# Kernel optimization log

Measured on AMD Instinct MI355X. Metric: run time of the kernel, lower is better.

## Reference

```python
import jax, jax.numpy as jnp
import numpy as np

D_MODEL = 1024
NUM_HEADS = 4
KEY_DIM = 1024      # dim * expand_k
VALUE_DIM = 2048    # dim * expand_v
HEAD_QK = KEY_DIM // NUM_HEADS   # 256
HEAD_V = VALUE_DIM // NUM_HEADS  # 512
EPS = 1e-5
ROPE_BASE = 10000.0
XAVIER_GAIN = 2.0 ** (-2.5)


def _xavier_uniform(key, shape, gain=XAVIER_GAIN):
    fan_in, fan_out = shape
    a = gain * np.sqrt(6.0 / (fan_in + fan_out))
    return jax.random.uniform(key, shape, jnp.float32, -a, a)


def setup_inputs() -> dict:
    key = jax.random.key(0)
    ks = jax.random.split(key, 5)
    x = jax.random.normal(ks[0], (2, 2048, D_MODEL), jnp.float32)
    # stored as (in, out); y = x @ W matches torch Linear(no bias) with W^T
    Wq = _xavier_uniform(ks[1], (D_MODEL, KEY_DIM))
    Wk = _xavier_uniform(ks[2], (D_MODEL, KEY_DIM))
    Wv = _xavier_uniform(ks[3], (D_MODEL, VALUE_DIM))
    Wo = _xavier_uniform(ks[4], (VALUE_DIM, D_MODEL))
    return {"x": x, "Wq": Wq, "Wk": Wk, "Wv": Wv, "Wo": Wo}


def _rope(t, base=ROPE_BASE):
    # t: [b, n, h, d]; standard half-split rotary embedding
    n, d = t.shape[1], t.shape[-1]
    half = d // 2
    inv_freq = 1.0 / (base ** (jnp.arange(0, half, dtype=jnp.float32) * 2.0 / d))
    ang = jnp.arange(n, dtype=jnp.float32)[:, None] * inv_freq  # [n, d/2]
    cos = jnp.cos(ang)[None, :, None, :]
    sin = jnp.sin(ang)[None, :, None, :]
    t1, t2 = t[..., :half], t[..., half:]
    return jnp.concatenate([t1 * cos - t2 * sin, t2 * cos + t1 * sin], axis=-1)


def reference(x, Wq, Wk, Wv, Wo):
    b, n, _ = x.shape
    # projections: b n (h d) -> b (n) h d
    q = (x @ Wq).reshape(b, n, NUM_HEADS, HEAD_QK)
    k = (x @ Wk).reshape(b, n, NUM_HEADS, HEAD_QK)
    v = (x @ Wv).reshape(b, n, NUM_HEADS, HEAD_V).transpose(0, 2, 1, 3)  # b h n dv
    q = _rope(q).transpose(0, 2, 1, 3)  # b h n dk
    k = _rope(k).transpose(0, 2, 1, 3)
    scale = HEAD_QK ** (-0.5)
    exp_qk = jnp.tril(jnp.exp(jnp.einsum('bhid,bhjd->bhij', q, k) * scale))
    exp_kk = jnp.tril(jnp.exp(jnp.einsum('bhid,bhjd->bhij', k, k) * scale))
    A = exp_kk.astype(jnp.float32) + EPS * jnp.eye(n, dtype=jnp.float32)
    sol = jax.lax.linalg.triangular_solve(A, v.astype(jnp.float32),
                                          left_side=True, lower=True)
    o = exp_qk.astype(jnp.float32) @ sol                # b h n dv
    o = o.transpose(0, 2, 1, 3).reshape(b, n, VALUE_DIM)  # b n (h dv)
    return o.astype(x.dtype) @ Wo
```

## Files before the change

kernel.cpp:

```cpp
#include <hip/hip_runtime.h>
#include <hip/hip_bf16.h>
#include <math.h>

#define SEQ   2048
#define NROW  4096
#define DM    1024
#define LDQ   1024
#define LDV   2048
#define NBLK  16

typedef float  f32x4  __attribute__((ext_vector_type(4)));
typedef int    i32x4  __attribute__((ext_vector_type(4)));
typedef __bf16 bf16x8 __attribute__((ext_vector_type(8)));

#define MFMA(d, a, b) (d) = __builtin_amdgcn_mfma_f32_16x16x32_bf16((a), (b), (d), 0, 0, 0)

__device__ inline ushort f2bf(float f) {
  __hip_bfloat16 h = __float2bfloat16(f);
  return *(ushort*)&h;
}
__device__ inline float bf2f(ushort u) {
  return __uint_as_float((unsigned)u << 16);
}
__device__ inline void split2(float v, ushort& hi, ushort& lo) {
  hi = f2bf(v);
  lo = f2bf(v - bf2f(hi));
}
__device__ inline bf16x8 ldfrag(const ushort* p) { return *(const bf16x8*)p; }

__device__ inline void gload_lds16(const ushort* g, ushort* l) {
  __builtin_amdgcn_global_load_lds(
      (const __attribute__((address_space(1))) void*)g,
      (__attribute__((address_space(3))) void*)l, 16, 0, 0);
}

__global__ void pack_x_kernel(const float* __restrict__ X, ushort* __restrict__ P)
{
  const int t = blockIdx.x * 256 + threadIdx.x;
  const int kc = t & 127;
  const int m  = t >> 7;
  const float* src = X + (size_t)m * DM + kc * 8;
  f32x4 v0 = *(const f32x4*)src;
  f32x4 v1 = *(const f32x4*)(src + 4);
  ushort o[8];
  #pragma unroll
  for (int j = 0; j < 4; ++j) { o[j] = f2bf(v0[j]); o[4 + j] = f2bf(v1[j]); }
  ushort* dst = P + ((size_t)((m >> 7) * 128 + kc) * 128 + (m & 127)) * 8;
  *(i32x4*)dst = *(i32x4*)o;
}

__global__ void pack_w_kernel(const float* __restrict__ W, ushort* __restrict__ P,
                              int K, int N)
{
  const int K8 = K >> 3;
  const int t = blockIdx.x * 256 + threadIdx.x;
  const int c  = t & 127;
  const int kc = (t >> 7) % K8;
  const int nb = t / (128 * K8);
  ushort o[8];
  #pragma unroll
  for (int j = 0; j < 8; ++j)
    o[j] = f2bf(W[(size_t)(kc * 8 + j) * N + nb * 128 + c]);
  ushort* dst = P + ((size_t)(nb * K8 + kc) * 128 + c) * 8;
  *(i32x4*)dst = *(i32x4*)o;
}

__global__ void rope_pack1_kernel(const float* __restrict__ M,
                                  ushort* __restrict__ Phi, ushort* __restrict__ Plo)
{
  const int idx = blockIdx.x * 256 + threadIdx.x;
  const int g   = idx & 31;
  const int h   = (idx >> 5) & 3;
  const int row = idx >> 7;
  const int pos = row & (SEQ - 1);
  const int d0  = g * 8;
  const bool hihalf = d0 >= 128;
  const int f0 = d0 & 127;
  const float* mp = M + (size_t)row * LDQ + h * 256;
  ushort oh[8], ol[8];
  #pragma unroll
  for (int j = 0; j < 8; ++j) {
    const int f = f0 + j;
    const float inv = expf(-(float)f * (9.210340371976184f / 128.f));
    float s, c;
    sincosf((float)pos * inv, &s, &c);
    const float m1 = mp[f], m2 = mp[f + 128];
    const float mv = hihalf ? (m2 * c + m1 * s) : (m1 * c - m2 * s);
    split2(mv, oh[j], ol[j]);
  }
  const int b = row >> 11, r = row & 127, tb = (row & 2047) >> 7;
  const int bh = b * 4 + h;
  const size_t doff = (((size_t)(bh * 16 + tb) * 32 + g) * 128 + r) * 8;
  *(i32x4*)(Phi + doff) = *(i32x4*)oh;
  *(i32x4*)(Plo + doff) = *(i32x4*)ol;
}

__global__ void pack_sol_kernel(const float* __restrict__ Vb, ushort* __restrict__ Sp)
{
  const int hj = blockIdx.x;
  const int h  = hj >> 4, jb = hj & 15;
  const int c  = blockIdx.y * 256 + threadIdx.x;
  const float* src = Vb + (size_t)(jb * 128) * LDV + h * 512 + c;
  ushort* dhi = Sp + ((size_t)hj * 2    ) * 65536;
  ushort* dlo = Sp + ((size_t)hj * 2 + 1) * 65536;
  for (int kc = 0; kc < 16; ++kc) {
    ushort oh[8], ol[8];
    #pragma unroll
    for (int j = 0; j < 8; ++j)
      split2(src[(size_t)(kc * 8 + j) * LDV], oh[j], ol[j]);
    *(i32x4*)(dhi + ((size_t)kc * 512 + c) * 8) = *(i32x4*)oh;
    *(i32x4*)(dlo + ((size_t)kc * 512 + c) * 8) = *(i32x4*)ol;
  }
}

__global__ __launch_bounds__(256) void gemm_bf16(
    const ushort* __restrict__ Ap, const ushort* __restrict__ Bp,
    float* __restrict__ C, int M, int N, int K)
{
  __shared__ __align__(16) ushort a_lds[8][128][8];
  __shared__ __align__(16) ushort b_lds[8][128][8];
  const int tid  = threadIdx.x;
  const int lane = tid & 63;
  const int w    = tid >> 6;
  const int wr   = w >> 1, wc = w & 1;
  const int mb = blockIdx.y, nb = blockIdx.x;
  const int K8 = K >> 3;
  const ushort* aT = Ap + (size_t)mb * K8 * 1024;
  const ushort* bT = Bp + (size_t)nb * K8 * 1024;
  const int lr = lane & 15;
  const int lk = lane >> 4;

  f32x4 acc[4][4];
  #pragma unroll
  for (int i = 0; i < 4; ++i)
    #pragma unroll
    for (int j = 0; j < 4; ++j) acc[i][j] = (f32x4)(0.f);

  for (int kc0 = 0; kc0 < K8; kc0 += 8) {
    const ushort* asrc = aT + (size_t)kc0 * 1024;
    const ushort* bsrc = bT + (size_t)kc0 * 1024;
    __syncthreads();
    #pragma unroll
    for (int it = 0; it < 4; ++it) {
      gload_lds16(asrc + it * 2048 + tid * 8, ((ushort*)a_lds) + it * 2048 + tid * 8);
      gload_lds16(bsrc + it * 2048 + tid * 8, ((ushort*)b_lds) + it * 2048 + tid * 8);
    }
    __syncthreads();
    #pragma unroll
    for (int kk = 0; kk < 2; ++kk) {
      bf16x8 af[4], bf[4];
      #pragma unroll
      for (int m = 0; m < 4; ++m)
        af[m] = ldfrag(&a_lds[kk * 4 + lk][wr * 64 + m * 16 + lr][0]);
      #pragma unroll
      for (int n = 0; n < 4; ++n)
        bf[n] = ldfrag(&b_lds[kk * 4 + lk][wc * 64 + n * 16 + lr][0]);
      #pragma unroll
      for (int m = 0; m < 4; ++m)
        #pragma unroll
        for (int n = 0; n < 4; ++n)
          MFMA(acc[m][n], af[m], bf[n]);
    }
  }
  const int r0 = (lane >> 4) * 4;
  #pragma unroll
  for (int m = 0; m < 4; ++m)
    #pragma unroll
    for (int n = 0; n < 4; ++n) {
      const int row = mb * 128 + wr * 64 + m * 16 + r0;
      const int col = nb * 128 + wc * 64 + n * 16 + lr;
      float* cp = C + (size_t)row * N + col;
      #pragma unroll
      for (int q = 0; q < 4; ++q) cp[(size_t)q * N] = acc[m][n][q];
    }
}

__global__ __launch_bounds__(256) void winv_kernel(
    const ushort* __restrict__ Khi, const ushort* __restrict__ Klo,
    ushort* __restrict__ Whi, ushort* __restrict__ Wlo)
{
  __shared__ float L[128][129];
  __shared__ float W[128][129];
  const int t = blockIdx.x, bh = blockIdx.y;
  const int tid = threadIdx.x;
  const int lane = tid & 63, w = tid >> 6;
  const int wr = w >> 1, wc = w & 1;
  const int lr = lane & 15, lk = lane >> 4;
  const size_t kb = (size_t)(bh * 16 + t) * 32768;

  f32x4 acc[4][4];
  #pragma unroll
  for (int i = 0; i < 4; ++i)
    #pragma unroll
    for (int j = 0; j < 4; ++j) acc[i][j] = (f32x4)(0.f);
  #pragma unroll
  for (int ks = 0; ks < 8; ++ks) {
    bf16x8 ah[4], al[4];
    #pragma unroll
    for (int m = 0; m < 4; ++m) {
      const size_t off = kb + ((size_t)(ks * 4 + lk) * 128 + wr * 64 + m * 16 + lr) * 8;
      ah[m] = ldfrag(Khi + off);
      al[m] = ldfrag(Klo + off);
    }
    #pragma unroll
    for (int n = 0; n < 4; ++n) {
      const size_t off = kb + ((size_t)(ks * 4 + lk) * 128 + wc * 64 + n * 16 + lr) * 8;
      bf16x8 bh_ = ldfrag(Khi + off);
      bf16x8 bl_ = ldfrag(Klo + off);
      #pragma unroll
      for (int m = 0; m < 4; ++m) {
        MFMA(acc[m][n], ah[m], bh_);
        MFMA(acc[m][n], ah[m], bl_);
        MFMA(acc[m][n], al[m], bh_);
      }
    }
  }
  for (int i = tid; i < 128 * 129; i += 256) ((float*)W)[i] = 0.f;
  #pragma unroll
  for (int m = 0; m < 4; ++m)
    #pragma unroll
    for (int n = 0; n < 4; ++n)
      #pragma unroll
      for (int q = 0; q < 4; ++q) {
        const int row = wr * 64 + m * 16 + lk * 4 + q;
        const int col = wc * 64 + n * 16 + lr;
        float v = __expf(acc[m][n][q] * 0.0625f);
        if (row == col) v += 1e-5f;
        L[row][col] = v;
      }
  __syncthreads();
  if (tid < 128) {
    const int c = tid;
    W[c][c] = 1.f / L[c][c];
    for (int r = c + 1; r < 128; ++r) {
      float s0 = 0.f, s1 = 0.f, s2 = 0.f, s3 = 0.f;
      int j = c;
      for (; j + 4 <= r; j += 4) {
        s0 += L[r][j]     * W[j][c];
        s1 += L[r][j + 1] * W[j + 1][c];
        s2 += L[r][j + 2] * W[j + 2][c];
        s3 += L[r][j + 3] * W[j + 3][c];
      }
      for (; j < r; ++j) s0 += L[r][j] * W[j][c];
      W[r][c] = -((s0 + s1) + (s2 + s3)) / L[r][r];
    }
  }
  __syncthreads();
  const size_t wb = (size_t)(bh * 16 + t) * 16384;
  for (int i = tid; i < 2048; i += 256) {
    const int kc = i >> 7, r = i & 127;
    ushort oh[8], ol[8];
    #pragma unroll
    for (int j = 0; j < 8; ++j) split2(W[r][kc * 8 + j], oh[j], ol[j]);
    *(i32x4*)(Whi + wb + (size_t)i * 8) = *(i32x4*)oh;
    *(i32x4*)(Wlo + wb + (size_t)i * 8) = *(i32x4*)ol;
  }
}

__global__ __launch_bounds__(512) void apply_w0_kernel(
    const ushort* __restrict__ Whi, const ushort* __restrict__ Wlo,
    float* __restrict__ V, ushort* __restrict__ SR)
{
  __shared__ __align__(16) ushort shi[16 * 128 * 8];
  __shared__ __align__(16) ushort slo[16 * 128 * 8];
  const int cc = blockIdx.x, bh = blockIdx.y;
  const int b = bh >> 2, h = bh & 3;
  const int tid = threadIdx.x;
  const int lane = tid & 63, w = tid >> 6;
  const int wr = w >> 2, wc = w & 3, lr = lane & 15, lk = lane >> 4;
  const size_t wb = (size_t)(bh * 16) * 16384;
  float* Vrows = V + (size_t)b * SEQ * LDV + h * 512;
  ushort* srw = SR + (size_t)bh * 131072;

  {
    const int k = tid >> 2, c0 = (tid & 3) * 32;
    const float* vp = Vrows + (size_t)k * LDV + cc * 128 + c0;
    for (int c = 0; c < 32; ++c) {
      ushort hi, lo;
      split2(vp[c], hi, lo);
      const int idx = (((k >> 3) * 128) + c0 + c) * 8 + (k & 7);
      shi[idx] = hi; slo[idx] = lo;
    }
  }
  __syncthreads();
  f32x4 acc[4][2];
  #pragma unroll
  for (int i = 0; i < 4; ++i)
    #pragma unroll
    for (int j = 0; j < 2; ++j) acc[i][j] = (f32x4)(0.f);
  #pragma unroll
  for (int ks = 0; ks < 4; ++ks) {
    bf16x8 ah[4], al[4];
    #pragma unroll
    for (int m = 0; m < 4; ++m) {
      const size_t off = wb + ((size_t)(ks * 4 + lk) * 128 + wr * 64 + m * 16 + lr) * 8;
      ah[m] = ldfrag(Whi + off);
      al[m] = ldfrag(Wlo + off);
    }
    #pragma unroll
    for (int n = 0; n < 2; ++n) {
      const int idx = (((ks * 4 + lk) * 128) + wc * 32 + n * 16 + lr) * 8;
      bf16x8 bh_ = ldfrag(&shi[idx]);
      bf16x8 bl_ = ldfrag(&slo[idx]);
      #pragma unroll
      for (int m = 0; m < 4; ++m) {
        MFMA(acc[m][n], ah[m], bh_);
        MFMA(acc[m][n], ah[m], bl_);
        MFMA(acc[m][n], al[m], bh_);
      }
    }
  }
  #pragma unroll
  for (int m = 0; m < 4; ++m)
    #pragma unroll
    for (int n = 0; n < 2; ++n) {
      const int col = wc * 32 + n * 16 + lr;
      #pragma unroll
      for (int q = 0; q < 4; ++q) {
        const int row = wr * 64 + m * 16 + lk * 4 + q;
        const float v = acc[m][n][q];
        Vrows[(size_t)row * LDV + cc * 128 + col] = v;
        ushort hi, lo;
        split2(v, hi, lo);
        const size_t so = ((size_t)(row >> 3) * 512 + cc * 128 + col) * 8 + (row & 7);
        srw[so] = hi; srw[65536 + so] = lo;
      }
    }
}

__global__ __launch_bounds__(512) void solve_step_kernel(
    const ushort* __restrict__ Khi, const ushort* __restrict__ Klo,
    const ushort* __restrict__ Whi, const ushort* __restrict__ Wlo,
    float* __restrict__ V, ushort* __restrict__ SR, int t)
{
  __shared__ __align__(16) ushort pAhi[16 * 128 * 8];
  __shared__ __align__(16) ushort pAlo[16 * 128 * 8];
  const int ib = t + 1 + blockIdx.x;
  const int cc = blockIdx.y;
  const int bh = blockIdx.z;
  const int b = bh >> 2, h = bh & 3;
  const bool lead = (blockIdx.x == 0);
  const int tid = threadIdx.x;
  const int lane = tid & 63, w = tid >> 6;
  const int wr = w >> 2, wc = w & 3, lr = lane & 15, lk = lane >> 4;
  const size_t kbi = (size_t)(bh * 16 + ib) * 32768;
  const size_t kbt = (size_t)(bh * 16 + t) * 32768;
  float* Vhead = V + (size_t)b * SEQ * LDV + h * 512;
  float* Vib = Vhead + (size_t)ib * 128 * LDV;
  const ushort* srr = SR + (size_t)(t & 1) * 1048576 + (size_t)bh * 131072;
  ushort* srw       = SR + (size_t)((t + 1) & 1) * 1048576 + (size_t)bh * 131072;

  {
    f32x4 a1[4][2];
    #pragma unroll
    for (int i = 0; i < 4; ++i)
      #pragma unroll
      for (int j = 0; j < 2; ++j) a1[i][j] = (f32x4)(0.f);
    #pragma unroll
    for (int ks = 0; ks < 8; ++ks) {
      bf16x8 ah[4], al[4];
      #pragma unroll
      for (int m = 0; m < 4; ++m) {
        const size_t off = kbi + ((size_t)(ks * 4 + lk) * 128 + wr * 64 + m * 16 + lr) * 8;
        ah[m] = ldfrag(Khi + off);
        al[m] = ldfrag(Klo + off);
      }
      #pragma unroll
      for (int n = 0; n < 2; ++n) {
        const size_t off = kbt + ((size_t)(ks * 4 + lk) * 128 + wc * 32 + n * 16 + lr) * 8;
        bf16x8 bh_ = ldfrag(Khi + off);
        bf16x8 bl_ = ldfrag(Klo + off);
        #pragma unroll
        for (int m = 0; m < 4; ++m) {
          MFMA(a1[m][n], ah[m], bh_);
          MFMA(a1[m][n], ah[m], bl_);
          MFMA(a1[m][n], al[m], bh_);
        }
      }
    }
    #pragma unroll
    for (int m = 0; m < 4; ++m)
      #pragma unroll
      for (int n = 0; n < 2; ++n)
        #pragma unroll
        for (int q = 0; q < 4; ++q) {
          const int row = wr * 64 + m * 16 + lk * 4 + q;
          const int c   = wc * 32 + n * 16 + lr;
          const float e = __expf(a1[m][n][q] * 0.0625f);
          ushort hi, lo;
          split2(e, hi, lo);
          const int idx = (((c >> 3) * 128) + row) * 8 + (c & 7);
          pAhi[idx] = hi; pAlo[idx] = lo;
        }
  }
  __syncthreads();

  f32x4 u[4][2];
  #pragma unroll
  for (int i = 0; i < 4; ++i)
    #pragma unroll
    for (int j = 0; j < 2; ++j) u[i][j] = (f32x4)(0.f);
  #pragma unroll
  for (int ks = 0; ks < 4; ++ks) {
    bf16x8 ah[4], al[4];
    #pragma unroll
    for (int m = 0; m < 4; ++m) {
      const int idx = (((ks * 4 + lk) * 128) + wr * 64 + m * 16 + lr) * 8;
      ah[m] = ldfrag(&pAhi[idx]);
      al[m] = ldfrag(&pAlo[idx]);
    }
    #pragma unroll
    for (int n = 0; n < 2; ++n) {
      const size_t c = cc * 128 + wc * 32 + n * 16 + lr;
      bf16x8 bh_ = ldfrag(srr + ((size_t)(ks * 4 + lk) * 512 + c) * 8);
      bf16x8 bl_ = ldfrag(srr + 65536 + ((size_t)(ks * 4 + lk) * 512 + c) * 8);
      #pragma unroll
      for (int m = 0; m < 4; ++m) {
        MFMA(u[m][n], ah[m], bh_);
        MFMA(u[m][n], ah[m], bl_);
        MFMA(u[m][n], al[m], bh_);
      }
    }
  }
  float nv[4][2][4];
  #pragma unroll
  for (int m = 0; m < 4; ++m)
    #pragma unroll
    for (int n = 0; n < 2; ++n) {
      const int col = wc * 32 + n * 16 + lr;
      #pragma unroll
      for (int q = 0; q < 4; ++q) {
        const int row = wr * 64 + m * 16 + lk * 4 + q;
        const float v = Vib[(size_t)row * LDV + cc * 128 + col] - u[m][n][q];
        nv[m][n][q] = v;
        if (!lead) Vib[(size_t)row * LDV + cc * 128 + col] = v;
      }
    }
  if (lead) {
    __syncthreads();
    #pragma unroll
    for (int m = 0; m < 4; ++m)
      #pragma unroll
      for (int n = 0; n < 2; ++n) {
        const int col = wc * 32 + n * 16 + lr;
        #pragma unroll
        for (int q = 0; q < 4; ++q) {
          const int row = wr * 64 + m * 16 + lk * 4 + q;
          ushort hi, lo;
          split2(nv[m][n][q], hi, lo);
          const int idx = (((row >> 3) * 128) + col) * 8 + (row & 7);
          pAhi[idx] = hi; pAlo[idx] = lo;
        }
      }
    __syncthreads();
    f32x4 s2[4][2];
    #pragma unroll
    for (int i = 0; i < 4; ++i)
      #pragma unroll
      for (int j = 0; j < 2; ++j) s2[i][j] = (f32x4)(0.f);
    const size_t wb = (size_t)(bh * 16 + ib) * 16384;
    #pragma unroll
    for (int ks = 0; ks < 4; ++ks) {
      bf16x8 ah[4], al[4];
      #pragma unroll
      for (int m = 0; m < 4; ++m) {
        const size_t off = wb + ((size_t)(ks * 4 + lk) * 128 + wr * 64 + m * 16 + lr) * 8;
        ah[m] = ldfrag(Whi + off);
        al[m] = ldfrag(Wlo + off);
      }
      #pragma unroll
      for (int n = 0; n < 2; ++n) {
        const int idx = (((ks * 4 + lk) * 128) + wc * 32 + n * 16 + lr) * 8;
        bf16x8 bh_ = ldfrag(&pAhi[idx]);
        bf16x8 bl_ = ldfrag(&pAlo[idx]);
        #pragma unroll
        for (int m = 0; m < 4; ++m) {
          MFMA(s2[m][n], ah[m], bh_);
          MFMA(s2[m][n], ah[m], bl_);
          MFMA(s2[m][n], al[m], bh_);
        }
      }
    }
    #pragma unroll
    for (int m = 0; m < 4; ++m)
      #pragma unroll
      for (int n = 0; n < 2; ++n) {
        const int col = wc * 32 + n * 16 + lr;
        #pragma unroll
        for (int q = 0; q < 4; ++q) {
          const int row = wr * 64 + m * 16 + lk * 4 + q;
          const float v = s2[m][n][q];
          Vib[(size_t)row * LDV + cc * 128 + col] = v;
          ushort hi, lo;
          split2(v, hi, lo);
          const size_t so = ((size_t)(row >> 3) * 512 + cc * 128 + col) * 8 + (row & 7);
          srw[so] = hi; srw[65536 + so] = lo;
        }
      }
  }
}

__global__ __launch_bounds__(512, 4) void o_kernel(
    const ushort* __restrict__ Qhi, const ushort* __restrict__ Qlo,
    const ushort* __restrict__ Khi, const ushort* __restrict__ Klo,
    const ushort* __restrict__ Sp0, const ushort* __restrict__ Sp1,
    ushort* __restrict__ Opack)
{
  __shared__ __align__(16) ushort Phi_s[16 * 64 * 8];
  __shared__ __align__(16) ushort Plo_s[16 * 64 * 8];
  const int bid = blockIdx.x;
  const int bh  = bid & 7;
  const int t3  = bid >> 3;
  const int ch  = t3 & 1;
  const int rh  = (t3 >> 1) & 1;
  const int ib  = 15 - (t3 >> 2);
  const int b = bh >> 2, h = bh & 3;
  const int tid = threadIdx.x;
  const int lane = tid & 63, w = tid >> 6;
  const int wr = w >> 2, wc = w & 3, lr = lane & 15, lk = lane >> 4;
  const ushort* Spb = b ? Sp1 : Sp0;

  const size_t qb = (size_t)(bh * 16 + ib) * 32768;
  f32x4 acc[2][4];
  #pragma unroll
  for (int i = 0; i < 2; ++i)
    #pragma unroll
    for (int j = 0; j < 4; ++j) acc[i][j] = (f32x4)(0.f);

  for (int jb = 0; jb <= ib; ++jb) {
    f32x4 s1[2][2];
    #pragma unroll
    for (int i = 0; i < 2; ++i)
      #pragma unroll
      for (int j = 0; j < 2; ++j) s1[i][j] = (f32x4)(0.f);
    const size_t kb = (size_t)(bh * 16 + jb) * 32768;
    __builtin_amdgcn_s_setprio(1);
    #pragma unroll
    for (int ks = 0; ks < 8; ++ks) {
      bf16x8 ah[2], al[2];
      #pragma unroll
      for (int m = 0; m < 2; ++m) {
        const size_t off = qb + ((size_t)(ks * 4 + lk) * 128 + rh * 64 + wr * 32 + m * 16 + lr) * 8;
        ah[m] = ldfrag(Qhi + off);
        al[m] = ldfrag(Qlo + off);
      }
      #pragma unroll
      for (int n = 0; n < 2; ++n) {
        const size_t off = kb + ((size_t)(ks * 4 + lk) * 128 + wc * 32 + n * 16 + lr) * 8;
        bf16x8 bh_ = ldfrag(Khi + off);
        bf16x8 bl_ = ldfrag(Klo + off);
        #pragma unroll
        for (int m = 0; m < 2; ++m) {
          MFMA(s1[m][n], ah[m], bh_);
          MFMA(s1[m][n], ah[m], bl_);
          MFMA(s1[m][n], al[m], bh_);
        }
      }
    }
    __builtin_amdgcn_s_setprio(0);
    if (jb) __syncthreads();
    #pragma unroll
    for (int m = 0; m < 2; ++m)
      #pragma unroll
      for (int n = 0; n < 2; ++n)
        #pragma unroll
        for (int q = 0; q < 4; ++q) {
          const int rloc = wr * 32 + m * 16 + lk * 4 + q;
          const int c    = wc * 32 + n * 16 + lr;
          float e = __expf(s1[m][n][q] * 0.0625f);
          if (jb == ib && c > rh * 64 + rloc) e = 0.f;
          ushort hi, lo;
          split2(e, hi, lo);
          const int idx = (((c >> 3) * 64) + rloc) * 8 + (c & 7);
          Phi_s[idx] = hi; Plo_s[idx] = lo;
        }
    __syncthreads();
    const ushort* sjb = Spb + ((size_t)(h * 16 + jb) * 2) * 65536;
    __builtin_amdgcn_s_setprio(1);
    #pragma unroll
    for (int ks = 0; ks < 4; ++ks) {
      bf16x8 ah[2], al[2];
      #pragma unroll
      for (int m = 0; m < 2; ++m) {
        const int idx = (((ks * 4 + lk) * 64) + wr * 32 + m * 16 + lr) * 8;
        ah[m] = ldfrag(&Phi_s[idx]);
        al[m] = ldfrag(&Plo_s[idx]);
      }
      #pragma unroll
      for (int n = 0; n < 4; ++n) {
        const size_t c = ch * 256 + wc * 64 + n * 16 + lr;
        bf16x8 bh_ = ldfrag(sjb + ((size_t)(ks * 4 + lk) * 512 + c) * 8);
        bf16x8 bl_ = ldfrag(sjb + 65536 + ((size_t)(ks * 4 + lk) * 512 + c) * 8);
        #pragma unroll
        for (int m = 0; m < 2; ++m) {
          MFMA(acc[m][n], ah[m], bh_);
          MFMA(acc[m][n], ah[m], bl_);
          MFMA(acc[m][n], al[m], bh_);
        }
      }
    }
    __builtin_amdgcn_s_setprio(0);
  }
  const int row_blk = b * 16 + ib;
  #pragma unroll
  for (int m = 0; m < 2; ++m)
    #pragma unroll
    for (int n = 0; n < 4; ++n) {
      const int col = h * 512 + ch * 256 + wc * 64 + n * 16 + lr;
      #pragma unroll
      for (int q = 0; q < 4; ++q) {
        const int row = rh * 64 + wr * 32 + m * 16 + lk * 4 + q;
        Opack[((size_t)row_blk * 256 + (col >> 3)) * 1024 + row * 8 + (col & 7)] =
            f2bf(acc[m][n][q]);
      }
    }
}

extern "C" void kernel_launch(void* const* d_in, const int* in_sizes, int n_in,
                              void* d_out, int out_size, void* d_ws, size_t ws_size,
                              hipStream_t stream)
{
  const float* x  = (const float*)d_in[0];
  const float* Wq = (const float*)d_in[1];
  const float* Wk = (const float*)d_in[2];
  const float* Wv = (const float*)d_in[3];
  const float* Wo = (const float*)d_in[4];
  float* out = (float*)d_out;

  char* base = (char*)d_ws;
  ushort* xpack = (ushort*)(base);
  ushort* Wqp   = (ushort*)(base + (8u  << 20));
  ushort* Wkp   = (ushort*)(base + (10u << 20));
  ushort* Wvp   = (ushort*)(base + (12u << 20));
  ushort* Wop   = (ushort*)(base + (16u << 20));
  float*  Q     = (float*) (base + (20u << 20));
  float*  K     = (float*) (base + (36u << 20));
  float*  V     = (float*) (base + (52u << 20));
  ushort* Qhi   = (ushort*)(base);
  ushort* Qlo   = (ushort*)(base + (8u  << 20));
  ushort* Khi   = (ushort*)(base + (20u << 20));
  ushort* Klo   = (ushort*)(base + (28u << 20));
  ushort* Whi   = (ushort*)(base + (36u << 20));
  ushort* Wlo   = (ushort*)(base + (40u << 20));
  ushort* SR    = (ushort*)(base + (44u << 20));
  ushort* Sp1   = (ushort*)(base + (36u << 20));
  ushort* Sp0   = (ushort*)(base + (68u << 20));
  ushort* Opack = (ushort*)(base + (52u << 20));

  pack_x_kernel<<<(NROW * 128) / 256, 256, 0, stream>>>(x, xpack);
  pack_w_kernel<<<(1024 * 1024 / 8) / 256, 256, 0, stream>>>(Wq, Wqp, 1024, 1024);
  pack_w_kernel<<<(1024 * 1024 / 8) / 256, 256, 0, stream>>>(Wk, Wkp, 1024, 1024);
  pack_w_kernel<<<(1024 * 2048 / 8) / 256, 256, 0, stream>>>(Wv, Wvp, 1024, 2048);
  pack_w_kernel<<<(2048 * 1024 / 8) / 256, 256, 0, stream>>>(Wo, Wop, 2048, 1024);

  gemm_bf16<<<dim3(DM / 128, NROW / 128), 256, 0, stream>>>(xpack, Wqp, Q, NROW, DM, DM);
  gemm_bf16<<<dim3(DM / 128, NROW / 128), 256, 0, stream>>>(xpack, Wkp, K, NROW, DM, DM);
  gemm_bf16<<<dim3(LDV / 128, NROW / 128), 256, 0, stream>>>(xpack, Wvp, V, NROW, LDV, DM);

  rope_pack1_kernel<<<(NROW * 4 * 32) / 256, 256, 0, stream>>>(Q, Qhi, Qlo);
  rope_pack1_kernel<<<(NROW * 4 * 32) / 256, 256, 0, stream>>>(K, Khi, Klo);

  winv_kernel<<<dim3(NBLK, 8), 256, 0, stream>>>(Khi, Klo, Whi, Wlo);
  apply_w0_kernel<<<dim3(4, 8), 512, 0, stream>>>(Whi, Wlo, V, SR);
  for (int t = 0; t < NBLK - 1; ++t)
    solve_step_kernel<<<dim3(NBLK - 1 - t, 4, 8), 512, 0, stream>>>(Khi, Klo, Whi, Wlo, V, SR, t);

  pack_sol_kernel<<<dim3(64, 2), 256, 0, stream>>>(V + (size_t)SEQ * LDV, Sp1);
  pack_sol_kernel<<<dim3(64, 2), 256, 0, stream>>>(V, Sp0);

  o_kernel<<<512, 512, 0, stream>>>(Qhi, Qlo, Khi, Klo, Sp0, Sp1, Opack);

  gemm_bf16<<<dim3(DM / 128, NROW / 128), 256, 0, stream>>>(Opack, Wop, out, NROW, DM, LDV);
}
```

Measured before the change: 1.296 ms.

## Split o_kernel into smaller 256-thread blocks with double-buffered P tile

```diff
diff --git a/kernel.cpp b/kernel.cpp
--- a/kernel.cpp
+++ b/kernel.cpp
@@ -500,24 +500,24 @@
   }
 }
 
-__global__ __launch_bounds__(512, 4) void o_kernel(
+__global__ __launch_bounds__(256, 4) void o_kernel(
     const ushort* __restrict__ Qhi, const ushort* __restrict__ Qlo,
     const ushort* __restrict__ Khi, const ushort* __restrict__ Klo,
     const ushort* __restrict__ Sp0, const ushort* __restrict__ Sp1,
     ushort* __restrict__ Opack)
 {
-  __shared__ __align__(16) ushort Phi_s[16 * 64 * 8];
-  __shared__ __align__(16) ushort Plo_s[16 * 64 * 8];
+  __shared__ __align__(16) ushort Phi_s[2][16 * 32 * 8];
+  __shared__ __align__(16) ushort Plo_s[2][16 * 32 * 8];
   const int bid = blockIdx.x;
   const int bh  = bid & 7;
-  const int t3  = bid >> 3;
-  const int ch  = t3 & 1;
-  const int rh  = (t3 >> 1) & 1;
-  const int ib  = 15 - (t3 >> 2);
+  const int rh  = (bid >> 3) & 3;
+  const int ch  = (bid >> 5) & 1;
+  const int ib  = 15 - (bid >> 6);
   const int b = bh >> 2, h = bh & 3;
   const int tid = threadIdx.x;
-  const int lane = tid & 63, w = tid >> 6;
-  const int wr = w >> 2, wc = w & 3, lr = lane & 15, lk = lane >> 4;
+  const int lane = tid & 63;
+  const int wv = tid >> 6;
+  const int lr = lane & 15, lk = lane >> 4;
   const ushort* Spb = b ? Sp1 : Sp0;
 
   const size_t qb = (size_t)(bh * 16 + ib) * 32768;
@@ -527,6 +527,7 @@
     #pragma unroll
     for (int j = 0; j < 4; ++j) acc[i][j] = (f32x4)(0.f);
 
+  int pb = 0;
   for (int jb = 0; jb <= ib; ++jb) {
     f32x4 s1[2][2];
     #pragma unroll
@@ -540,13 +541,13 @@
       bf16x8 ah[2], al[2];
       #pragma unroll
       for (int m = 0; m < 2; ++m) {
-        const size_t off = qb + ((size_t)(ks * 4 + lk) * 128 + rh * 64 + wr * 32 + m * 16 + lr) * 8;
+        const size_t off = qb + ((size_t)(ks * 4 + lk) * 128 + rh * 32 + m * 16 + lr) * 8;
         ah[m] = ldfrag(Qhi + off);
         al[m] = ldfrag(Qlo + off);
       }
       #pragma unroll
       for (int n = 0; n < 2; ++n) {
-        const size_t off = kb + ((size_t)(ks * 4 + lk) * 128 + wc * 32 + n * 16 + lr) * 8;
+        const size_t off = kb + ((size_t)(ks * 4 + lk) * 128 + wv * 32 + n * 16 + lr) * 8;
         bf16x8 bh_ = ldfrag(Khi + off);
         bf16x8 bl_ = ldfrag(Klo + off);
         #pragma unroll
@@ -558,21 +559,20 @@
       }
     }
     __builtin_amdgcn_s_setprio(0);
-    if (jb) __syncthreads();
     #pragma unroll
     for (int m = 0; m < 2; ++m)
       #pragma unroll
       for (int n = 0; n < 2; ++n)
         #pragma unroll
         for (int q = 0; q < 4; ++q) {
-          const int rloc = wr * 32 + m * 16 + lk * 4 + q;
-          const int c    = wc * 32 + n * 16 + lr;
+          const int rloc = m * 16 + lk * 4 + q;
+          const int c    = wv * 32 + n * 16 + lr;
           float e = __expf(s1[m][n][q] * 0.0625f);
-          if (jb == ib && c > rh * 64 + rloc) e = 0.f;
+          if (jb == ib && c > rh * 32 + rloc) e = 0.f;
           ushort hi, lo;
           split2(e, hi, lo);
-          const int idx = (((c >> 3) * 64) + rloc) * 8 + (c & 7);
-          Phi_s[idx] = hi; Plo_s[idx] = lo;
+          const int idx = (((c >> 3) * 32) + rloc) * 8 + (c & 7);
+          Phi_s[pb][idx] = hi; Plo_s[pb][idx] = lo;
         }
     __syncthreads();
     const ushort* sjb = Spb + ((size_t)(h * 16 + jb) * 2) * 65536;
@@ -582,13 +582,13 @@
       bf16x8 ah[2], al[2];
       #pragma unroll
       for (int m = 0; m < 2; ++m) {
-        const int idx = (((ks * 4 + lk) * 64) + wr * 32 + m * 16 + lr) * 8;
-        ah[m] = ldfrag(&Phi_s[idx]);
-        al[m] = ldfrag(&Plo_s[idx]);
+        const int idx = (((ks * 4 + lk) * 32) + m * 16 + lr) * 8;
+        ah[m] = ldfrag(&Phi_s[pb][idx]);
+        al[m] = ldfrag(&Plo_s[pb][idx]);
       }
       #pragma unroll
       for (int n = 0; n < 4; ++n) {
-        const size_t c = ch * 256 + wc * 64 + n * 16 + lr;
+        const size_t c = ch * 256 + wv * 64 + n * 16 + lr;
         bf16x8 bh_ = ldfrag(sjb + ((size_t)(ks * 4 + lk) * 512 + c) * 8);
         bf16x8 bl_ = ldfrag(sjb + 65536 + ((size_t)(ks * 4 + lk) * 512 + c) * 8);
         #pragma unroll
@@ -600,16 +600,17 @@
       }
     }
     __builtin_amdgcn_s_setprio(0);
+    pb ^= 1;
   }
   const int row_blk = b * 16 + ib;
   #pragma unroll
   for (int m = 0; m < 2; ++m)
     #pragma unroll
     for (int n = 0; n < 4; ++n) {
-      const int col = h * 512 + ch * 256 + wc * 64 + n * 16 + lr;
+      const int col = h * 512 + ch * 256 + wv * 64 + n * 16 + lr;
       #pragma unroll
       for (int q = 0; q < 4; ++q) {
-        const int row = rh * 64 + wr * 32 + m * 16 + lk * 4 + q;
+        const int row = rh * 32 + m * 16 + lk * 4 + q;
         Opack[((size_t)row_blk * 256 + (col >> 3)) * 1024 + row * 8 + (col & 7)] =
             f2bf(acc[m][n][q]);
       }
@@ -668,7 +669,7 @@
   pack_sol_kernel<<<dim3(64, 2), 256, 0, stream>>>(V + (size_t)SEQ * LDV, Sp1);
   pack_sol_kernel<<<dim3(64, 2), 256, 0, stream>>>(V, Sp0);
 
-  o_kernel<<<512, 512, 0, stream>>>(Qhi, Qlo, Khi, Klo, Sp0, Sp1, Opack);
+  o_kernel<<<1024, 256, 0, stream>>>(Qhi, Qlo, Khi, Klo, Sp0, Sp1, Opack);
 
   gemm_bf16<<<dim3(DM / 128, NROW / 128), 256, 0, stream>>>(Opack, Wop, out, NROW, DM, LDV);
 }
```

Result: faster. 1.270 ms (-2.0%).
